# Optimization experiments

Hardware: AMD Instinct MI355X
Metric: run time of the kernel (lower is better)

The kernel has to match this reference:

```python
import jax, jax.numpy as jnp
import numpy as np

N_NODES = 100000
N_EDGES = 1600000
F_IN = 128
F_EDGE = 16
HID = 64


def gcn_conv(x, W, b, src, dst, n):
    # PyG GCNConv: add self-loops, symmetric normalization D^-1/2 (A+I) D^-1/2
    h = x @ W  # [N, out]
    loop = jnp.arange(n, dtype=src.dtype)
    src_f = jnp.concatenate([src, loop])
    dst_f = jnp.concatenate([dst, loop])
    ones = jnp.ones(src_f.shape[0], dtype=h.dtype)
    deg = jax.ops.segment_sum(ones, dst_f, num_segments=n)
    dinv = jnp.where(deg > 0, jax.lax.rsqrt(deg), 0.0)
    norm = dinv[src_f] * dinv[dst_f]  # [E+N]
    msg = h[src_f] * norm[:, None]
    out = jax.ops.segment_sum(msg, dst_f, num_segments=n)
    return out + b


def setup_inputs() -> dict:
    key = jax.random.key(0)
    ks = jax.random.split(key, 16)
    g = lambda k, shape, fan_in: jax.random.normal(k, shape, dtype=jnp.float32) * (1.0 / np.sqrt(fan_in))
    inp = {
        "x": jax.random.normal(ks[0], (N_NODES, F_IN), dtype=jnp.float32),
        "edge_index": jax.random.randint(ks[1], (2, N_EDGES), 0, N_NODES, dtype=jnp.int64) if jax.config.read('jax_enable_x64') else jax.random.randint(ks[1], (2, N_EDGES), 0, N_NODES, dtype=jnp.int32),
        "edge_attr": jax.random.normal(ks[2], (N_EDGES, F_EDGE), dtype=jnp.float32),
        # GCN layers
        "W1": g(ks[3], (F_IN, HID), F_IN), "b1": jnp.zeros((HID,), jnp.float32),
        "W2": g(ks[4], (HID, HID), HID), "b2": jnp.zeros((HID,), jnp.float32),
        "W3": g(ks[5], (HID, HID), HID), "b3": jnp.zeros((HID,), jnp.float32),
        # edge MLP: Linear(2*HID+F_EDGE -> HID), Linear(HID -> 32), Linear(32 -> 2)
        "Wm1": g(ks[6], (2 * HID + F_EDGE, HID), 2 * HID + F_EDGE), "bm1": jnp.zeros((HID,), jnp.float32),
        "Wm2": g(ks[7], (HID, 32), HID), "bm2": jnp.zeros((32,), jnp.float32),
        "Wm3": g(ks[8], (32, 2), 32), "bm3": jnp.zeros((2,), jnp.float32),
    }
    return inp


def reference(x, edge_index, edge_attr, W1, b1, W2, b2, W3, b3, Wm1, bm1, Wm2, bm2, Wm3, bm3):
    src, dst = edge_index[0], edge_index[1]
    n = x.shape[0]
    h = jax.nn.relu(gcn_conv(x, W1, b1, src, dst, n))
    h = jax.nn.relu(gcn_conv(h, W2, b2, src, dst, n))
    h = jax.nn.relu(gcn_conv(h, W3, b3, src, dst, n))
    # edge classifier: gather endpoints, concat edge features, small MLP (eval mode -> no dropout)
    e = jnp.concatenate([h[src], h[dst], edge_attr], axis=1)  # [E, 2*HID+F_EDGE]
    e = jax.nn.relu(e @ Wm1 + bm1)
    e = jax.nn.relu(e @ Wm2 + bm2)
    return e @ Wm3 + bm3  # [E, 2]
```

## Files before the change

### kernel.cpp

```cpp
#include <hip/hip_runtime.h>

typedef __attribute__((ext_vector_type(8))) short bf16x8;
typedef __attribute__((ext_vector_type(4))) float f32x4;
typedef __attribute__((ext_vector_type(4))) unsigned int u32x4;

__device__ __forceinline__ short f2bf(float f) {
  unsigned u = __float_as_uint(f);
  u = (u + 0x7fffu + ((u >> 16) & 1u)) >> 16;
  return (short)u;
}
__device__ __forceinline__ float bf2f(unsigned short u) {
  return __uint_as_float(((unsigned)u) << 16);
}
__device__ __forceinline__ unsigned cvtpk(float lo, float hi) {
  unsigned r;
  asm("v_cvt_pk_bf16_f32 %0, %1, %2" : "=v"(r) : "v"(lo), "v"(hi));
  return r;
}
__device__ __forceinline__ bf16x8 u2b(u32x4 w) {
  union { u32x4 u; bf16x8 b; } x; x.u = w; return x.b;
}

__global__ __launch_bounds__(256) void fill_pad_k(const int* __restrict__ src,
                                                  const int* __restrict__ dst,
                                                  unsigned* cursor,
                                                  int* __restrict__ csr_pad, int e, int n) {
  const int part  = blockIdx.x & 7;
  const int lo    = (int)(((long)n * part) >> 3);
  const int hi    = (int)(((long)n * (part + 1)) >> 3);
  const int nb    = gridDim.x >> 3;
  const int brank = blockIdx.x >> 3;
  const long stride = (long)nb * 256;
  const int e4 = e >> 2;
  const int4* dst4 = (const int4*)dst;
  for (long i = (long)brank * 256 + threadIdx.x; i < e4; i += stride) {
    int4 d = dst4[i];
    long eb = i * 4;
    if (d.x >= lo && d.x < hi) { int p = (int)atomicAdd(&cursor[d.x], 1u); if (p < 64) csr_pad[((size_t)d.x << 6) + p] = src[eb]; }
    if (d.y >= lo && d.y < hi) { int p = (int)atomicAdd(&cursor[d.y], 1u); if (p < 64) csr_pad[((size_t)d.y << 6) + p] = src[eb + 1]; }
    if (d.z >= lo && d.z < hi) { int p = (int)atomicAdd(&cursor[d.z], 1u); if (p < 64) csr_pad[((size_t)d.z << 6) + p] = src[eb + 2]; }
    if (d.w >= lo && d.w < hi) { int p = (int)atomicAdd(&cursor[d.w], 1u); if (p < 64) csr_pad[((size_t)d.w << 6) + p] = src[eb + 3]; }
  }
  for (long i = (long)e4 * 4 + (long)brank * 256 + threadIdx.x; i < e; i += stride) {
    int d = dst[i];
    if (d >= lo && d < hi) { int p = (int)atomicAdd(&cursor[d], 1u); if (p < 64) csr_pad[((size_t)d << 6) + p] = src[i]; }
  }
}

__global__ void dinv_k(const unsigned* __restrict__ deg, float* __restrict__ dinv, int n) {
  int i = blockIdx.x * 256 + threadIdx.x;
  if (i < n) dinv[i] = rsqrtf((float)(deg[i] + 1u));
}

__global__ void pack_all_k(const float* __restrict__ W1, const float* __restrict__ W2,
                           const float* __restrict__ W3, const float* __restrict__ Wm1,
                           const float* __restrict__ Wm2,
                           short* __restrict__ Wn1p, short* __restrict__ Wn2p,
                           short* __restrict__ Wn3p, short* __restrict__ We1p,
                           short* __restrict__ We2p) {
  const int t = blockIdx.x * 256 + threadIdx.x;
  const int stride = gridDim.x * 256;
  auto pack64 = [&](const float* W, short* P, int K, int total) {
    for (int i = t; i < total; i += stride) {
      int j = i & 7, l = (i >> 3) & 63, c = (i >> 9) & 3, kk = i >> 11;
      int row = kk * 32 + ((l >> 4) * 8) + j, col = c * 16 + (l & 15);
      P[i] = f2bf(row < K ? W[row * 64 + col] : 0.f);
    }
  };
  pack64(W1, Wn1p, 128, 8192);
  pack64(W2, Wn2p, 64, 4096);
  pack64(W3, Wn3p, 64, 4096);
  for (int i = t; i < 10240; i += stride) {
    int j = i & 7, l = (i >> 3) & 63, c = (i >> 9) & 3, kk = i >> 11;
    int row = kk * 32 + ((l >> 4) * 8) + j;
    int r_ = l & 15;
    int col = 32 * (c >> 1) + 8 * (r_ >> 2) + 4 * (c & 1) + (r_ & 3);
    We1p[i] = f2bf(row < 144 ? Wm1[row * 64 + col] : 0.f);
  }
  for (int i = t; i < 2048; i += stride) {
    int j = i & 7, l = (i >> 3) & 63, c = (i >> 9) & 1, kk = (i >> 10) & 1;
    int row = kk * 32 + ((l >> 4) * 8) + j, col = c * 16 + (l & 15);
    We2p[i] = f2bf(Wm2[row * 32 + col]);
  }
}

template<int K, bool F32IN>
__global__ __launch_bounds__(256) void node_mfma_k(
    const void* __restrict__ Araw, const short* __restrict__ Wp,
    unsigned short* __restrict__ C, int n)
{
  constexpr int NK = K / 32;
  __shared__ __align__(16) short Wl[NK * 4 * 64 * 8];
  const int tid = threadIdx.x;
  {
    const uint4* s = (const uint4*)Wp; uint4* d = (uint4*)Wl;
    for (int i = tid; i < NK * 4 * 64; i += 256) d[i] = s[i];
  }
  __syncthreads();
  const int lane = tid & 63;
  const int wid  = tid >> 6;
  const int g    = lane >> 4;
  const int r16  = lane & 15;
  const int base = blockIdx.x * 64 + wid * 16;
  if (base >= n) return;
  int arow = base + r16;
  if (arow >= n) arow = n - 1;
  const bf16x8* wb = (const bf16x8*)Wl;
  f32x4 acc[4];
  #pragma unroll
  for (int c = 0; c < 4; ++c) acc[c] = (f32x4){0.f, 0.f, 0.f, 0.f};
  #pragma unroll
  for (int kk = 0; kk < NK; ++kk) {
    bf16x8 a;
    if (F32IN) {
      const float4* af = (const float4*)((const float*)Araw + (size_t)arow * K + kk * 32 + 8 * g);
      float4 u = af[0], v = af[1];
      u32x4 w;
      w[0] = cvtpk(u.x, u.y); w[1] = cvtpk(u.z, u.w);
      w[2] = cvtpk(v.x, v.y); w[3] = cvtpk(v.z, v.w);
      a = u2b(w);
    } else {
      a = ((const bf16x8*)((const unsigned short*)Araw + (size_t)arow * K))[kk * 4 + g];
    }
    #pragma unroll
    for (int c = 0; c < 4; ++c)
      acc[c] = __builtin_amdgcn_mfma_f32_16x16x32_bf16(a, wb[(kk * 4 + c) * 64 + lane], acc[c], 0, 0, 0);
  }
  #pragma unroll
  for (int rr = 0; rr < 4; ++rr) {
    int orow = base + g * 4 + rr;
    if (orow < n) {
      unsigned short* cp = C + (size_t)orow * 64 + r16;
      cp[0]  = (unsigned short)f2bf(acc[0][rr]);
      cp[16] = (unsigned short)f2bf(acc[1][rr]);
      cp[32] = (unsigned short)f2bf(acc[2][rr]);
      cp[48] = (unsigned short)f2bf(acc[3][rr]);
    }
  }
}

__global__ __launch_bounds__(256) void agg_csr_k(
    const unsigned short* __restrict__ lin, const float* __restrict__ dinv,
    const unsigned* __restrict__ deg, const int* __restrict__ csr_pad,
    const float* __restrict__ bias, unsigned short* __restrict__ out, int n)
{
  const int node = blockIdx.x * 4 + (threadIdx.x >> 6);
  if (node >= n) return;
  const int lane = threadIdx.x & 63;
  const int es = lane >> 4;
  const int fq = lane & 15;
  const float dn = dinv[node];
  const int cnt = (int)deg[node];
  const int* sp = csr_pad + ((size_t)node << 6);
  float ax = 0.f, ay = 0.f, az = 0.f, aw = 0.f;
  if (es == 0) {
    ushort4 v = *(const ushort4*)(lin + (size_t)node * 64 + fq * 4);
    float w = dn * dn;
    ax = w * bf2f(v.x); ay = w * bf2f(v.y); az = w * bf2f(v.z); aw = w * bf2f(v.w);
  }
  #pragma unroll 4
  for (int j = es; j < cnt; j += 4) {
    int s = sp[j];
    float w = dinv[s] * dn;
    ushort4 v = *(const ushort4*)(lin + (size_t)s * 64 + fq * 4);
    ax += w * bf2f(v.x); ay += w * bf2f(v.y);
    az += w * bf2f(v.z); aw += w * bf2f(v.w);
  }
  ax += __shfl_xor(ax, 16, 64); ax += __shfl_xor(ax, 32, 64);
  ay += __shfl_xor(ay, 16, 64); ay += __shfl_xor(ay, 32, 64);
  az += __shfl_xor(az, 16, 64); az += __shfl_xor(az, 32, 64);
  aw += __shfl_xor(aw, 16, 64); aw += __shfl_xor(aw, 32, 64);
  if (es == 0) {
    float4 b = *(const float4*)(bias + fq * 4);
    ushort4 o;
    o.x = (unsigned short)f2bf(fmaxf(ax + b.x, 0.f));
    o.y = (unsigned short)f2bf(fmaxf(ay + b.y, 0.f));
    o.z = (unsigned short)f2bf(fmaxf(az + b.z, 0.f));
    o.w = (unsigned short)f2bf(fmaxf(aw + b.w, 0.f));
    *(ushort4*)(out + (size_t)node * 64 + fq * 4) = o;
  }
}

__global__ __launch_bounds__(256) void agg_gemm_k(
    const unsigned short* __restrict__ h_in, const float* __restrict__ dinv,
    const unsigned* __restrict__ deg, const int* __restrict__ csr_pad,
    const short* __restrict__ Wp, const float* __restrict__ bias,
    unsigned short* __restrict__ h_out, int n)
{
  __shared__ __align__(16) short Wl[4096];
  __shared__ __align__(16) short X[4][16][72];
  const int tid = threadIdx.x;
  {
    const uint4* s = (const uint4*)Wp; uint4* d = (uint4*)Wl;
    for (int i = tid; i < 512; i += 256) d[i] = s[i];
  }
  const int lane = tid & 63;
  const int wid  = tid >> 6;
  const int es   = lane >> 4;
  const int fq   = lane & 15;
  const int base = blockIdx.x * 64 + wid * 16;

  for (int nd = 0; nd < 16; ++nd) {
    int node = base + nd;
    if (node >= n) node = n - 1;
    const float dn = dinv[node];
    const int cnt = (int)deg[node];
    const int* sp = csr_pad + ((size_t)node << 6);
    float ax = 0.f, ay = 0.f, az = 0.f, aw = 0.f;
    if (es == 0) {
      ushort4 v = *(const ushort4*)(h_in + (size_t)node * 64 + fq * 4);
      float w = dn * dn;
      ax = w * bf2f(v.x); ay = w * bf2f(v.y); az = w * bf2f(v.z); aw = w * bf2f(v.w);
    }
    #pragma unroll 4
    for (int j = es; j < cnt; j += 4) {
      int s = sp[j];
      float w = dinv[s] * dn;
      ushort4 v = *(const ushort4*)(h_in + (size_t)s * 64 + fq * 4);
      ax += w * bf2f(v.x); ay += w * bf2f(v.y);
      az += w * bf2f(v.z); aw += w * bf2f(v.w);
    }
    ax += __shfl_xor(ax, 16, 64); ax += __shfl_xor(ax, 32, 64);
    ay += __shfl_xor(ay, 16, 64); ay += __shfl_xor(ay, 32, 64);
    az += __shfl_xor(az, 16, 64); az += __shfl_xor(az, 32, 64);
    aw += __shfl_xor(aw, 16, 64); aw += __shfl_xor(aw, 32, 64);
    if (es == 0) {
      ushort4 o;
      o.x = (unsigned short)f2bf(ax); o.y = (unsigned short)f2bf(ay);
      o.z = (unsigned short)f2bf(az); o.w = (unsigned short)f2bf(aw);
      *(ushort4*)&X[wid][nd][fq * 4] = o;
    }
  }
  __syncthreads();

  const int g = es, r16 = fq;
  float bcol[4];
  #pragma unroll
  for (int c = 0; c < 4; ++c) bcol[c] = bias[c * 16 + r16];
  const bf16x8* wb = (const bf16x8*)Wl;
  f32x4 acc[4];
  #pragma unroll
  for (int c = 0; c < 4; ++c) acc[c] = (f32x4){bcol[c], bcol[c], bcol[c], bcol[c]};
  #pragma unroll
  for (int kk = 0; kk < 2; ++kk) {
    bf16x8 a = *(const bf16x8*)&X[wid][r16][kk * 32 + 8 * g];
    #pragma unroll
    for (int c = 0; c < 4; ++c)
      acc[c] = __builtin_amdgcn_mfma_f32_16x16x32_bf16(a, wb[(kk * 4 + c) * 64 + lane], acc[c], 0, 0, 0);
  }
  #pragma unroll
  for (int rr = 0; rr < 4; ++rr) {
    int orow = base + g * 4 + rr;
    if (orow < n) {
      unsigned short* cp = h_out + (size_t)orow * 64 + r16;
      cp[0]  = (unsigned short)f2bf(fmaxf(acc[0][rr], 0.f));
      cp[16] = (unsigned short)f2bf(fmaxf(acc[1][rr], 0.f));
      cp[32] = (unsigned short)f2bf(fmaxf(acc[2][rr], 0.f));
      cp[48] = (unsigned short)f2bf(fmaxf(acc[3][rr], 0.f));
    }
  }
}

__global__ __launch_bounds__(256) void edge_mlp_mfma_k(
    const unsigned short* __restrict__ hb, const float* __restrict__ ea,
    const int* __restrict__ src, const int* __restrict__ dst,
    const short* __restrict__ W1p, const short* __restrict__ W2p,
    const float* __restrict__ bm1, const float* __restrict__ bm2,
    const float* __restrict__ Wm3, const float* __restrict__ bm3,
    float* __restrict__ out, int E, int ntiles)
{
  const int tid  = threadIdx.x;
  const int lane = tid & 63;
  const int wid  = tid >> 6;
  const int g    = lane >> 4;
  const int r16  = lane & 15;

  bf16x8 w1f[20];
  #pragma unroll
  for (int t = 0; t < 20; ++t) w1f[t] = ((const bf16x8*)W1p)[t * 64 + lane];
  bf16x8 w2f[4];
  #pragma unroll
  for (int t = 0; t < 4; ++t) w2f[t] = ((const bf16x8*)W2p)[t * 64 + lane];

  f32x4 b1v[4];
  #pragma unroll
  for (int c = 0; c < 4; ++c) {
    float4 v = *(const float4*)(bm1 + 32 * (c >> 1) + 8 * g + 4 * (c & 1));
    b1v[c] = (f32x4){v.x, v.y, v.z, v.w};
  }
  f32x4 b2v[2];
  #pragma unroll
  for (int c = 0; c < 2; ++c) {
    float4 v = *(const float4*)(bm2 + c * 16 + 4 * g);
    b2v[c] = (f32x4){v.x, v.y, v.z, v.w};
  }
  float4 w3a[2], w3b[2];
  #pragma unroll
  for (int c = 0; c < 2; ++c) {
    w3a[c] = *(const float4*)(Wm3 + (c * 16 + 4 * g) * 2);
    w3b[c] = *(const float4*)(Wm3 + (c * 16 + 4 * g) * 2 + 4);
  }
  const float b30 = bm3[0], b31 = bm3[1];

  const int ngroups = (ntiles + 3) >> 2;
  if (blockIdx.x >= ngroups) return;

  int mye1, sl1, dl1;
  bf16x8 c_a0, c_a1, c_a2, c_a3;
  float4 c_e0, c_e1;
  {
    int e = (blockIdx.x * 4 + wid) * 16 + r16;
    int mye = (e < E) ? e : (E - 1);
    int sl = src[mye], dl = dst[mye];
    const bf16x8* hs = (const bf16x8*)(hb + (size_t)sl * 64);
    c_a0 = hs[g]; c_a1 = hs[4 + g];
    const bf16x8* hd = (const bf16x8*)(hb + (size_t)dl * 64);
    c_a2 = hd[g]; c_a3 = hd[4 + g];
    if (g < 2) {
      const float4* ep = (const float4*)(ea + (size_t)mye * 16 + 8 * g);
      c_e0 = ep[0]; c_e1 = ep[1];
    }
    int grp1 = blockIdx.x + gridDim.x;
    if (grp1 > ngroups - 1) grp1 = ngroups - 1;
    int e1 = (grp1 * 4 + wid) * 16 + r16;
    mye1 = (e1 < E) ? e1 : (E - 1);
    sl1 = src[mye1]; dl1 = dst[mye1];
  }

  for (int grp = blockIdx.x; grp < ngroups; grp += gridDim.x) {
    const int e0 = (grp * 4 + wid) * 16;

    bf16x8 n_a0, n_a1, n_a2, n_a3;
    float4 n_e0, n_e1;
    {
      const bf16x8* hs = (const bf16x8*)(hb + (size_t)sl1 * 64);
      n_a0 = hs[g]; n_a1 = hs[4 + g];
      const bf16x8* hd = (const bf16x8*)(hb + (size_t)dl1 * 64);
      n_a2 = hd[g]; n_a3 = hd[4 + g];
      if (g < 2) {
        const float4* ep = (const float4*)(ea + (size_t)mye1 * 16 + 8 * g);
        n_e0 = ep[0]; n_e1 = ep[1];
      }
    }
    int mye2, sl2, dl2;
    {
      int grp2 = grp + 2 * gridDim.x;
      if (grp2 > ngroups - 1) grp2 = ngroups - 1;
      int e2 = (grp2 * 4 + wid) * 16 + r16;
      mye2 = (e2 < E) ? e2 : (E - 1);
      sl2 = src[mye2]; dl2 = dst[mye2];
    }

    bf16x8 a4;
    if (g < 2) {
      u32x4 w;
      w[0] = cvtpk(c_e0.x, c_e0.y); w[1] = cvtpk(c_e0.z, c_e0.w);
      w[2] = cvtpk(c_e1.x, c_e1.y); w[3] = cvtpk(c_e1.z, c_e1.w);
      a4 = u2b(w);
    } else {
      a4 = (bf16x8){0, 0, 0, 0, 0, 0, 0, 0};
    }

    f32x4 acc[4];
    #pragma unroll
    for (int c = 0; c < 4; ++c) acc[c] = b1v[c];
    #pragma unroll
    for (int c = 0; c < 4; ++c) {
      acc[c] = __builtin_amdgcn_mfma_f32_16x16x32_bf16(w1f[0 * 4 + c], c_a0, acc[c], 0, 0, 0);
      acc[c] = __builtin_amdgcn_mfma_f32_16x16x32_bf16(w1f[1 * 4 + c], c_a1, acc[c], 0, 0, 0);
      acc[c] = __builtin_amdgcn_mfma_f32_16x16x32_bf16(w1f[2 * 4 + c], c_a2, acc[c], 0, 0, 0);
      acc[c] = __builtin_amdgcn_mfma_f32_16x16x32_bf16(w1f[3 * 4 + c], c_a3, acc[c], 0, 0, 0);
      acc[c] = __builtin_amdgcn_mfma_f32_16x16x32_bf16(w1f[4 * 4 + c], a4,   acc[c], 0, 0, 0);
    }

    u32x4 x0w, x1w;
    x0w[0] = cvtpk(fmaxf(acc[0][0], 0.f), fmaxf(acc[0][1], 0.f));
    x0w[1] = cvtpk(fmaxf(acc[0][2], 0.f), fmaxf(acc[0][3], 0.f));
    x0w[2] = cvtpk(fmaxf(acc[1][0], 0.f), fmaxf(acc[1][1], 0.f));
    x0w[3] = cvtpk(fmaxf(acc[1][2], 0.f), fmaxf(acc[1][3], 0.f));
    x1w[0] = cvtpk(fmaxf(acc[2][0], 0.f), fmaxf(acc[2][1], 0.f));
    x1w[1] = cvtpk(fmaxf(acc[2][2], 0.f), fmaxf(acc[2][3], 0.f));
    x1w[2] = cvtpk(fmaxf(acc[3][0], 0.f), fmaxf(acc[3][1], 0.f));
    x1w[3] = cvtpk(fmaxf(acc[3][2], 0.f), fmaxf(acc[3][3], 0.f));
    bf16x8 xa0 = u2b(x0w), xa1 = u2b(x1w);

    f32x4 acc2[2];
    #pragma unroll
    for (int c = 0; c < 2; ++c) acc2[c] = b2v[c];
    #pragma unroll
    for (int c = 0; c < 2; ++c) {
      acc2[c] = __builtin_amdgcn_mfma_f32_16x16x32_bf16(w2f[0 * 2 + c], xa0, acc2[c], 0, 0, 0);
      acc2[c] = __builtin_amdgcn_mfma_f32_16x16x32_bf16(w2f[1 * 2 + c], xa1, acc2[c], 0, 0, 0);
    }

    float p0 = 0.f, p1 = 0.f;
    #pragma unroll
    for (int c = 0; c < 2; ++c) {
      float v0 = fmaxf(acc2[c][0], 0.f);
      float v1 = fmaxf(acc2[c][1], 0.f);
      float v2 = fmaxf(acc2[c][2], 0.f);
      float v3 = fmaxf(acc2[c][3], 0.f);
      p0 = fmaf(v0, w3a[c].x, p0); p1 = fmaf(v0, w3a[c].y, p1);
      p0 = fmaf(v1, w3a[c].z, p0); p1 = fmaf(v1, w3a[c].w, p1);
      p0 = fmaf(v2, w3b[c].x, p0); p1 = fmaf(v2, w3b[c].y, p1);
      p0 = fmaf(v3, w3b[c].z, p0); p1 = fmaf(v3, w3b[c].w, p1);
    }
    p0 += __shfl_xor(p0, 16, 64); p0 += __shfl_xor(p0, 32, 64);
    p1 += __shfl_xor(p1, 16, 64); p1 += __shfl_xor(p1, 32, 64);
    if (g == 0) {
      int e = e0 + r16;
      if (e < E) {
        float2 o; o.x = p0 + b30; o.y = p1 + b31;
        *(float2*)(out + (size_t)e * 2) = o;
      }
    }

    c_a0 = n_a0; c_a1 = n_a1; c_a2 = n_a2; c_a3 = n_a3;
    c_e0 = n_e0; c_e1 = n_e1;
    mye1 = mye2; sl1 = sl2; dl1 = dl2;
  }
}

extern "C" void kernel_launch(void* const* d_in, const int* in_sizes, int n_in,
                              void* d_out, int out_size, void* d_ws, size_t ws_size,
                              hipStream_t stream) {
  const float* x   = (const float*)d_in[0];
  const int*   ei  = (const int*)d_in[1];
  const float* ea  = (const float*)d_in[2];
  const float* W1  = (const float*)d_in[3];
  const float* b1  = (const float*)d_in[4];
  const float* W2  = (const float*)d_in[5];
  const float* b2  = (const float*)d_in[6];
  const float* W3  = (const float*)d_in[7];
  const float* b3  = (const float*)d_in[8];
  const float* Wm1 = (const float*)d_in[9];
  const float* bm1 = (const float*)d_in[10];
  const float* Wm2 = (const float*)d_in[11];
  const float* bm2 = (const float*)d_in[12];
  const float* Wm3 = (const float*)d_in[13];
  const float* bm3 = (const float*)d_in[14];

  const int N  = in_sizes[0] / 128;
  const int E  = in_sizes[1] / 2;
  const int* srcp = ei;
  const int* dstp = ei + E;

  float* ws = (float*)d_ws;
  size_t off = 0;
  float*    dinv    = ws + off;               off += (size_t)N;
  unsigned* cursor  = (unsigned*)(ws + off);  off += (size_t)N;
  int*      csr_pad = (int*)(ws + off);       off += (size_t)N * 64;
  unsigned short* lin = (unsigned short*)(ws + off); off += (size_t)N * 32;
  unsigned short* hA  = (unsigned short*)(ws + off); off += (size_t)N * 32;
  unsigned short* hB  = (unsigned short*)(ws + off); off += (size_t)N * 32;
  short* Wn1p = (short*)(ws + off); off += 4096;
  short* Wn2p = (short*)(ws + off); off += 2048;
  short* Wn3p = (short*)(ws + off); off += 2048;
  short* We1p = (short*)(ws + off); off += 5120;
  short* We2p = (short*)(ws + off); off += 1024;

  const int gN    = (N + 255) / 256;
  const int gNode = (N + 63) / 64;
  const int gAgg  = (N + 3) / 4;
  const int ntiles = (E + 15) / 16;

  hipMemsetAsync(cursor, 0, (size_t)N * 4, stream);

  fill_pad_k<<<2048, 256, 0, stream>>>(srcp, dstp, cursor, csr_pad, E, N);
  dinv_k<<<gN, 256, 0, stream>>>(cursor, dinv, N);
  pack_all_k<<<40, 256, 0, stream>>>(W1, W2, W3, Wm1, Wm2, Wn1p, Wn2p, Wn3p, We1p, We2p);

  node_mfma_k<128, true><<<gNode, 256, 0, stream>>>(x, Wn1p, lin, N);
  agg_csr_k<<<gAgg, 256, 0, stream>>>(lin, dinv, cursor, csr_pad, b1, hA, N);
  agg_gemm_k<<<gNode, 256, 0, stream>>>(hA, dinv, cursor, csr_pad, Wn2p, b2, hB, N);
  agg_gemm_k<<<gNode, 256, 0, stream>>>(hB, dinv, cursor, csr_pad, Wn3p, b3, hA, N);

  edge_mlp_mfma_k<<<2048, 256, 0, stream>>>(hA, ea, srcp, dstp, We1p, We2p,
      bm1, bm2, Wm3, bm3, (float*)d_out, E, ntiles);
}
```

Baseline: 361.4 us.

## Merge CSR fill, weight packing and first GEMM into one prep kernel; recompute dinv

Combines the CSR fill, the Wm1/Wm2 packing and the first node GEMM into one heterogeneous launch, with blocks split by blockIdx range so the independent stages run concurrently. The dinv kernel and buffer are removed: the aggregation kernels recompute rsqrt(deg+1) inline, and W2/W3 are converted to bf16 inside each agg_gemm block instead of being packed once ahead of time. This cuts four launches and lets the compute-bound GEMM overlap the atomic-bound fill. In exchange each block repeats the weight conversion, and every neighbor visit now does an extra rsqrt.

```diff
diff --git a/kernel.cpp b/kernel.cpp
--- a/kernel.cpp
+++ b/kernel.cpp
@@ -21,135 +21,113 @@
   union { u32x4 u; bf16x8 b; } x; x.u = w; return x.b;
 }
 
-__global__ __launch_bounds__(256) void fill_pad_k(const int* __restrict__ src,
-                                                  const int* __restrict__ dst,
-                                                  unsigned* cursor,
-                                                  int* __restrict__ csr_pad, int e, int n) {
-  const int part  = blockIdx.x & 7;
-  const int lo    = (int)(((long)n * part) >> 3);
-  const int hi    = (int)(((long)n * (part + 1)) >> 3);
-  const int nb    = gridDim.x >> 3;
-  const int brank = blockIdx.x >> 3;
-  const long stride = (long)nb * 256;
-  const int e4 = e >> 2;
-  const int4* dst4 = (const int4*)dst;
-  for (long i = (long)brank * 256 + threadIdx.x; i < e4; i += stride) {
-    int4 d = dst4[i];
-    long eb = i * 4;
-    if (d.x >= lo && d.x < hi) { int p = (int)atomicAdd(&cursor[d.x], 1u); if (p < 64) csr_pad[((size_t)d.x << 6) + p] = src[eb]; }
-    if (d.y >= lo && d.y < hi) { int p = (int)atomicAdd(&cursor[d.y], 1u); if (p < 64) csr_pad[((size_t)d.y << 6) + p] = src[eb + 1]; }
-    if (d.z >= lo && d.z < hi) { int p = (int)atomicAdd(&cursor[d.z], 1u); if (p < 64) csr_pad[((size_t)d.z << 6) + p] = src[eb + 2]; }
-    if (d.w >= lo && d.w < hi) { int p = (int)atomicAdd(&cursor[d.w], 1u); if (p < 64) csr_pad[((size_t)d.w << 6) + p] = src[eb + 3]; }
-  }
-  for (long i = (long)e4 * 4 + (long)brank * 256 + threadIdx.x; i < e; i += stride) {
-    int d = dst[i];
-    if (d >= lo && d < hi) { int p = (int)atomicAdd(&cursor[d], 1u); if (p < 64) csr_pad[((size_t)d << 6) + p] = src[i]; }
-  }
-}
-
-__global__ void dinv_k(const unsigned* __restrict__ deg, float* __restrict__ dinv, int n) {
-  int i = blockIdx.x * 256 + threadIdx.x;
-  if (i < n) dinv[i] = rsqrtf((float)(deg[i] + 1u));
-}
-
-__global__ void pack_all_k(const float* __restrict__ W1, const float* __restrict__ W2,
-                           const float* __restrict__ W3, const float* __restrict__ Wm1,
-                           const float* __restrict__ Wm2,
-                           short* __restrict__ Wn1p, short* __restrict__ Wn2p,
-                           short* __restrict__ Wn3p, short* __restrict__ We1p,
-                           short* __restrict__ We2p) {
-  const int t = blockIdx.x * 256 + threadIdx.x;
-  const int stride = gridDim.x * 256;
-  auto pack64 = [&](const float* W, short* P, int K, int total) {
-    for (int i = t; i < total; i += stride) {
+#define FILLB 2048
+#define PACKB 40
+
+__global__ __launch_bounds__(256) void prep_k(
+    const float* __restrict__ x, const float* __restrict__ W1,
+    const float* __restrict__ Wm1, const float* __restrict__ Wm2,
+    const int* __restrict__ src, const int* __restrict__ dst,
+    unsigned* cursor, int* __restrict__ csr_pad,
+    short* __restrict__ We1p, short* __restrict__ We2p,
+    unsigned short* __restrict__ lin, int e, int n, int nNodeB)
+{
+  __shared__ __align__(16) short Wl[8192];
+  const int tid = threadIdx.x;
+
+  if (blockIdx.x < FILLB) {
+    const int part  = blockIdx.x & 7;
+    const int lo    = (int)(((long)n * part) >> 3);
+    const int hi    = (int)(((long)n * (part + 1)) >> 3);
+    const int brank = blockIdx.x >> 3;
+    const long stride = (long)(FILLB >> 3) * 256;
+    const int e4 = e >> 2;
+    const int4* dst4 = (const int4*)dst;
+    for (long i = (long)brank * 256 + tid; i < e4; i += stride) {
+      int4 d = dst4[i];
+      long eb = i * 4;
+      if (d.x >= lo && d.x < hi) { int p = (int)atomicAdd(&cursor[d.x], 1u); if (p < 64) csr_pad[((size_t)d.x << 6) + p] = src[eb]; }
+      if (d.y >= lo && d.y < hi) { int p = (int)atomicAdd(&cursor[d.y], 1u); if (p < 64) csr_pad[((size_t)d.y << 6) + p] = src[eb + 1]; }
+      if (d.z >= lo && d.z < hi) { int p = (int)atomicAdd(&cursor[d.z], 1u); if (p < 64) csr_pad[((size_t)d.z << 6) + p] = src[eb + 2]; }
+      if (d.w >= lo && d.w < hi) { int p = (int)atomicAdd(&cursor[d.w], 1u); if (p < 64) csr_pad[((size_t)d.w << 6) + p] = src[eb + 3]; }
+    }
+    for (long i = (long)e4 * 4 + (long)brank * 256 + tid; i < e; i += stride) {
+      int d = dst[i];
+      if (d >= lo && d < hi) { int p = (int)atomicAdd(&cursor[d], 1u); if (p < 64) csr_pad[((size_t)d << 6) + p] = src[i]; }
+    }
+  } else if (blockIdx.x < FILLB + nNodeB) {
+    const int nb = blockIdx.x - FILLB;
+    for (int i = tid; i < 8192; i += 256) {
       int j = i & 7, l = (i >> 3) & 63, c = (i >> 9) & 3, kk = i >> 11;
       int row = kk * 32 + ((l >> 4) * 8) + j, col = c * 16 + (l & 15);
-      P[i] = f2bf(row < K ? W[row * 64 + col] : 0.f);
-    }
-  };
-  pack64(W1, Wn1p, 128, 8192);
-  pack64(W2, Wn2p, 64, 4096);
-  pack64(W3, Wn3p, 64, 4096);
-  for (int i = t; i < 10240; i += stride) {
-    int j = i & 7, l = (i >> 3) & 63, c = (i >> 9) & 3, kk = i >> 11;
-    int row = kk * 32 + ((l >> 4) * 8) + j;
-    int r_ = l & 15;
-    int col = 32 * (c >> 1) + 8 * (r_ >> 2) + 4 * (c & 1) + (r_ & 3);
-    We1p[i] = f2bf(row < 144 ? Wm1[row * 64 + col] : 0.f);
-  }
-  for (int i = t; i < 2048; i += stride) {
-    int j = i & 7, l = (i >> 3) & 63, c = (i >> 9) & 1, kk = (i >> 10) & 1;
-    int row = kk * 32 + ((l >> 4) * 8) + j, col = c * 16 + (l & 15);
-    We2p[i] = f2bf(Wm2[row * 32 + col]);
-  }
-}
-
-template<int K, bool F32IN>
-__global__ __launch_bounds__(256) void node_mfma_k(
-    const void* __restrict__ Araw, const short* __restrict__ Wp,
-    unsigned short* __restrict__ C, int n)
-{
-  constexpr int NK = K / 32;
-  __shared__ __align__(16) short Wl[NK * 4 * 64 * 8];
-  const int tid = threadIdx.x;
-  {
-    const uint4* s = (const uint4*)Wp; uint4* d = (uint4*)Wl;
-    for (int i = tid; i < NK * 4 * 64; i += 256) d[i] = s[i];
-  }
-  __syncthreads();
-  const int lane = tid & 63;
-  const int wid  = tid >> 6;
-  const int g    = lane >> 4;
-  const int r16  = lane & 15;
-  const int base = blockIdx.x * 64 + wid * 16;
-  if (base >= n) return;
-  int arow = base + r16;
-  if (arow >= n) arow = n - 1;
-  const bf16x8* wb = (const bf16x8*)Wl;
-  f32x4 acc[4];
-  #pragma unroll
-  for (int c = 0; c < 4; ++c) acc[c] = (f32x4){0.f, 0.f, 0.f, 0.f};
-  #pragma unroll
-  for (int kk = 0; kk < NK; ++kk) {
-    bf16x8 a;
-    if (F32IN) {
-      const float4* af = (const float4*)((const float*)Araw + (size_t)arow * K + kk * 32 + 8 * g);
-      float4 u = af[0], v = af[1];
-      u32x4 w;
-      w[0] = cvtpk(u.x, u.y); w[1] = cvtpk(u.z, u.w);
-      w[2] = cvtpk(v.x, v.y); w[3] = cvtpk(v.z, v.w);
-      a = u2b(w);
-    } else {
-      a = ((const bf16x8*)((const unsigned short*)Araw + (size_t)arow * K))[kk * 4 + g];
-    }
-    #pragma unroll
-    for (int c = 0; c < 4; ++c)
-      acc[c] = __builtin_amdgcn_mfma_f32_16x16x32_bf16(a, wb[(kk * 4 + c) * 64 + lane], acc[c], 0, 0, 0);
-  }
-  #pragma unroll
-  for (int rr = 0; rr < 4; ++rr) {
-    int orow = base + g * 4 + rr;
-    if (orow < n) {
-      unsigned short* cp = C + (size_t)orow * 64 + r16;
-      cp[0]  = (unsigned short)f2bf(acc[0][rr]);
-      cp[16] = (unsigned short)f2bf(acc[1][rr]);
-      cp[32] = (unsigned short)f2bf(acc[2][rr]);
-      cp[48] = (unsigned short)f2bf(acc[3][rr]);
+      Wl[i] = f2bf(W1[row * 64 + col]);
+    }
+    __syncthreads();
+    const int lane = tid & 63;
+    const int wid  = tid >> 6;
+    const int g    = lane >> 4;
+    const int r16  = lane & 15;
+    const int base = nb * 64 + wid * 16;
+    if (base < n) {
+      int arow = base + r16;
+      if (arow >= n) arow = n - 1;
+      const bf16x8* wb = (const bf16x8*)Wl;
+      f32x4 acc[4];
+      #pragma unroll
+      for (int c = 0; c < 4; ++c) acc[c] = (f32x4){0.f, 0.f, 0.f, 0.f};
+      #pragma unroll
+      for (int kk = 0; kk < 4; ++kk) {
+        const float4* af = (const float4*)(x + (size_t)arow * 128 + kk * 32 + 8 * g);
+        float4 u = af[0], v = af[1];
+        u32x4 w;
+        w[0] = cvtpk(u.x, u.y); w[1] = cvtpk(u.z, u.w);
+        w[2] = cvtpk(v.x, v.y); w[3] = cvtpk(v.z, v.w);
+        bf16x8 a = u2b(w);
+        #pragma unroll
+        for (int c = 0; c < 4; ++c)
+          acc[c] = __builtin_amdgcn_mfma_f32_16x16x32_bf16(a, wb[(kk * 4 + c) * 64 + lane], acc[c], 0, 0, 0);
+      }
+      #pragma unroll
+      for (int rr = 0; rr < 4; ++rr) {
+        int orow = base + g * 4 + rr;
+        if (orow < n) {
+          unsigned short* cp = lin + (size_t)orow * 64 + r16;
+          cp[0]  = (unsigned short)f2bf(acc[0][rr]);
+          cp[16] = (unsigned short)f2bf(acc[1][rr]);
+          cp[32] = (unsigned short)f2bf(acc[2][rr]);
+          cp[48] = (unsigned short)f2bf(acc[3][rr]);
+        }
+      }
+    }
+  } else {
+    const int t = (blockIdx.x - FILLB - nNodeB) * 256 + tid;
+    const int stride = PACKB * 256;
+    for (int i = t; i < 10240; i += stride) {
+      int j = i & 7, l = (i >> 3) & 63, c = (i >> 9) & 3, kk = i >> 11;
+      int row = kk * 32 + ((l >> 4) * 8) + j;
+      int r_ = l & 15;
+      int col = 32 * (c >> 1) + 8 * (r_ >> 2) + 4 * (c & 1) + (r_ & 3);
+      We1p[i] = f2bf(row < 144 ? Wm1[row * 64 + col] : 0.f);
+    }
+    for (int i = t; i < 2048; i += stride) {
+      int j = i & 7, l = (i >> 3) & 63, c = (i >> 9) & 1, kk = (i >> 10) & 1;
+      int row = kk * 32 + ((l >> 4) * 8) + j, col = c * 16 + (l & 15);
+      We2p[i] = f2bf(Wm2[row * 32 + col]);
     }
   }
 }
 
 __global__ __launch_bounds__(256) void agg_csr_k(
-    const unsigned short* __restrict__ lin, const float* __restrict__ dinv,
-    const unsigned* __restrict__ deg, const int* __restrict__ csr_pad,
-    const float* __restrict__ bias, unsigned short* __restrict__ out, int n)
+    const unsigned short* __restrict__ lin, const unsigned* __restrict__ deg,
+    const int* __restrict__ csr_pad, const float* __restrict__ bias,
+    unsigned short* __restrict__ out, int n)
 {
   const int node = blockIdx.x * 4 + (threadIdx.x >> 6);
   if (node >= n) return;
   const int lane = threadIdx.x & 63;
   const int es = lane >> 4;
   const int fq = lane & 15;
-  const float dn = dinv[node];
+  const float dn = rsqrtf((float)(deg[node] + 1u));
   const int cnt = (int)deg[node];
   const int* sp = csr_pad + ((size_t)node << 6);
   float ax = 0.f, ay = 0.f, az = 0.f, aw = 0.f;
@@ -161,7 +139,7 @@
   #pragma unroll 4
   for (int j = es; j < cnt; j += 4) {
     int s = sp[j];
-    float w = dinv[s] * dn;
+    float w = rsqrtf((float)(deg[s] + 1u)) * dn;
     ushort4 v = *(const ushort4*)(lin + (size_t)s * 64 + fq * 4);
     ax += w * bf2f(v.x); ay += w * bf2f(v.y);
     az += w * bf2f(v.z); aw += w * bf2f(v.w);
@@ -182,17 +160,17 @@
 }
 
 __global__ __launch_bounds__(256) void agg_gemm_k(
-    const unsigned short* __restrict__ h_in, const float* __restrict__ dinv,
-    const unsigned* __restrict__ deg, const int* __restrict__ csr_pad,
-    const short* __restrict__ Wp, const float* __restrict__ bias,
-    unsigned short* __restrict__ h_out, int n)
+    const unsigned short* __restrict__ h_in, const unsigned* __restrict__ deg,
+    const int* __restrict__ csr_pad, const float* __restrict__ W,
+    const float* __restrict__ bias, unsigned short* __restrict__ h_out, int n)
 {
   __shared__ __align__(16) short Wl[4096];
   __shared__ __align__(16) short X[4][16][72];
   const int tid = threadIdx.x;
-  {
-    const uint4* s = (const uint4*)Wp; uint4* d = (uint4*)Wl;
-    for (int i = tid; i < 512; i += 256) d[i] = s[i];
+  for (int i = tid; i < 4096; i += 256) {
+    int j = i & 7, l = (i >> 3) & 63, c = (i >> 9) & 3, kk = i >> 11;
+    int row = kk * 32 + ((l >> 4) * 8) + j, col = c * 16 + (l & 15);
+    Wl[i] = f2bf(W[row * 64 + col]);
   }
   const int lane = tid & 63;
   const int wid  = tid >> 6;
@@ -203,7 +181,7 @@
   for (int nd = 0; nd < 16; ++nd) {
     int node = base + nd;
     if (node >= n) node = n - 1;
-    const float dn = dinv[node];
+    const float dn = rsqrtf((float)(deg[node] + 1u));
     const int cnt = (int)deg[node];
     const int* sp = csr_pad + ((size_t)node << 6);
     float ax = 0.f, ay = 0.f, az = 0.f, aw = 0.f;
@@ -215,7 +193,7 @@
     #pragma unroll 4
     for (int j = es; j < cnt; j += 4) {
       int s = sp[j];
-      float w = dinv[s] * dn;
+      float w = rsqrtf((float)(deg[s] + 1u)) * dn;
       ushort4 v = *(const ushort4*)(h_in + (size_t)s * 64 + fq * 4);
       ax += w * bf2f(v.x); ay += w * bf2f(v.y);
       az += w * bf2f(v.z); aw += w * bf2f(v.w);
@@ -447,33 +425,26 @@
 
   float* ws = (float*)d_ws;
   size_t off = 0;
-  float*    dinv    = ws + off;               off += (size_t)N;
   unsigned* cursor  = (unsigned*)(ws + off);  off += (size_t)N;
   int*      csr_pad = (int*)(ws + off);       off += (size_t)N * 64;
   unsigned short* lin = (unsigned short*)(ws + off); off += (size_t)N * 32;
   unsigned short* hA  = (unsigned short*)(ws + off); off += (size_t)N * 32;
   unsigned short* hB  = (unsigned short*)(ws + off); off += (size_t)N * 32;
-  short* Wn1p = (short*)(ws + off); off += 4096;
-  short* Wn2p = (short*)(ws + off); off += 2048;
-  short* Wn3p = (short*)(ws + off); off += 2048;
   short* We1p = (short*)(ws + off); off += 5120;
   short* We2p = (short*)(ws + off); off += 1024;
 
-  const int gN    = (N + 255) / 256;
   const int gNode = (N + 63) / 64;
   const int gAgg  = (N + 3) / 4;
   const int ntiles = (E + 15) / 16;
 
   hipMemsetAsync(cursor, 0, (size_t)N * 4, stream);
 
-  fill_pad_k<<<2048, 256, 0, stream>>>(srcp, dstp, cursor, csr_pad, E, N);
-  dinv_k<<<gN, 256, 0, stream>>>(cursor, dinv, N);
-  pack_all_k<<<40, 256, 0, stream>>>(W1, W2, W3, Wm1, Wm2, Wn1p, Wn2p, Wn3p, We1p, We2p);
-
-  node_mfma_k<128, true><<<gNode, 256, 0, stream>>>(x, Wn1p, lin, N);
-  agg_csr_k<<<gAgg, 256, 0, stream>>>(lin, dinv, cursor, csr_pad, b1, hA, N);
-  agg_gemm_k<<<gNode, 256, 0, stream>>>(hA, dinv, cursor, csr_pad, Wn2p, b2, hB, N);
-  agg_gemm_k<<<gNode, 256, 0, stream>>>(hB, dinv, cursor, csr_pad, Wn3p, b3, hA, N);
+  prep_k<<<FILLB + gNode + PACKB, 256, 0, stream>>>(
+      x, W1, Wm1, Wm2, srcp, dstp, cursor, csr_pad, We1p, We2p, lin, E, N, gNode);
+
+  agg_csr_k<<<gAgg, 256, 0, stream>>>(lin, cursor, csr_pad, b1, hA, N);
+  agg_gemm_k<<<gNode, 256, 0, stream>>>(hA, cursor, csr_pad, W2, b2, hB, N);
+  agg_gemm_k<<<gNode, 256, 0, stream>>>(hB, cursor, csr_pad, W3, b3, hA, N);
 
   edge_mlp_mfma_k<<<2048, 256, 0, stream>>>(hA, ea, srcp, dstp, We1p, We2p,
       bm1, bm2, Wm3, bm3, (float*)d_out, E, ntiles);
```

Result: no change. 363.2 us (+0.5%).
